# Kernel tuning notes

Measured on AMD Instinct MI355X. Metric: run time of the kernel, lower is better.

Reference implementation:

```python
import jax, jax.numpy as jnp
import numpy as np

PE_DIM = 64

def _layernorm(x, g, b, eps=1e-5):
    m = jnp.mean(x, -1, keepdims=True)
    v = jnp.mean((x - m) ** 2, -1, keepdims=True)
    return (x - m) * jax.lax.rsqrt(v + eps) * g + b

def _sinusoidal_pe(t, dim=PE_DIM):
    half = dim // 2
    freqs = jnp.exp(-jnp.log(10000.0) * jnp.arange(half) / half).astype(t.dtype)
    ang = t[..., None] * freqs  # [..., half]
    return jnp.concatenate([jnp.sin(ang), jnp.cos(ang)], -1)

def _bilinear(feats, b, t, x, y):
    # feats [B,Wl,H,W,D]; b,t int32 [B,Q,Wl,M] (b broadcastable); x,y in [0,1]
    # matches torch grid_sample(mode=bilinear, padding_mode=border, align_corners=False)
    H, W = feats.shape[2], feats.shape[3]
    px = x * W - 0.5
    py = y * H - 0.5
    x0 = jnp.floor(px); y0 = jnp.floor(py)
    wx = (px - x0)[..., None]; wy = (py - y0)[..., None]
    x0i = jnp.clip(x0.astype(jnp.int32), 0, W - 1)
    x1i = jnp.clip(x0.astype(jnp.int32) + 1, 0, W - 1)
    y0i = jnp.clip(y0.astype(jnp.int32), 0, H - 1)
    y1i = jnp.clip(y0.astype(jnp.int32) + 1, 0, H - 1)
    v00 = feats[b, t, y0i, x0i]  # [B,Q,Wl,M,D]
    v01 = feats[b, t, y0i, x1i]
    v10 = feats[b, t, y1i, x0i]
    v11 = feats[b, t, y1i, x1i]
    return (v00 * (1 - wy) * (1 - wx) + v01 * (1 - wy) * wx
            + v10 * wy * (1 - wx) + v11 * wy * wx)

def setup_inputs() -> dict:
    key = jax.random.key(0)
    ks = jax.random.split(key, 20)
    B, Q, Wl, H, W, D, M = 4, 300, 8, 64, 64, 256, 4
    s = 0.02
    inp = {
        'q': jax.random.normal(ks[0], (B, Q, D), jnp.float32),
        'kv_feats': jax.random.normal(ks[1], (B, Wl, H, W, D), jnp.float32),
        'kv_mask': jnp.zeros((B, Wl, H, W), jnp.bool_),
        'delta_sec': jax.random.normal(ks[2], (B, Q, Wl), jnp.float32),
        'w_ref': jax.random.normal(ks[3], (D, 2), jnp.float32) * s,
        'b_ref': jnp.zeros((2,), jnp.float32),
        'w_delta': jax.random.normal(ks[4], (2 * D, 3 * M), jnp.float32) * s,
        'b_delta': jnp.zeros((3 * M,), jnp.float32),
        'w_alpha': jax.random.normal(ks[5], (2 * D, M), jnp.float32) * s,
        'b_alpha': jnp.zeros((M,), jnp.float32),
        'lam': jnp.array(1.0, jnp.float32),
        'w_proj': jax.random.normal(ks[6], (D, D), jnp.float32) * s,
        'b_proj': jnp.zeros((D,), jnp.float32),
        'ln1_g': jnp.ones((D,), jnp.float32), 'ln1_b': jnp.zeros((D,), jnp.float32),
        'ln2_g': jnp.ones((D,), jnp.float32), 'ln2_b': jnp.zeros((D,), jnp.float32),
        'w_ffn1': jax.random.normal(ks[7], (D, 4 * D), jnp.float32) * s,
        'b_ffn1': jnp.zeros((4 * D,), jnp.float32),
        'w_ffn2': jax.random.normal(ks[8], (4 * D, D), jnp.float32) * s,
        'b_ffn2': jnp.zeros((D,), jnp.float32),
        'w_rel': jax.random.normal(ks[9], (PE_DIM, D), jnp.float32) * s,
        'b_rel': jnp.zeros((D,), jnp.float32),
    }
    return inp

def reference(q, kv_feats, kv_mask, delta_sec, w_ref, b_ref, w_delta, b_delta,
              w_alpha, b_alpha, lam, w_proj, b_proj, ln1_g, ln1_b, ln2_g, ln2_b,
              w_ffn1, b_ffn1, w_ffn2, b_ffn2, w_rel, b_rel):
    B, Q, D = q.shape
    Wl = kv_feats.shape[1]
    M = w_alpha.shape[1]

    qn = _layernorm(q, ln1_g, ln1_b)
    rel_feat = _sinusoidal_pe(delta_sec) @ w_rel + b_rel          # [B,Q,Wl,D]
    psi = jnp.concatenate([jnp.broadcast_to(qn[:, :, None, :], (B, Q, Wl, D)),
                           rel_feat], -1)                          # [B,Q,Wl,2D]

    delta = (psi @ w_delta + b_delta).reshape(B, Q, Wl, M, 3)
    logits = psi @ w_alpha + b_alpha                               # [B,Q,Wl,M]
    ref = jax.nn.sigmoid(qn @ w_ref + b_ref)                       # [B,Q,2]
    coords = ref[:, :, None, None, :] + jnp.tanh(delta[..., :2])   # [B,Q,Wl,M,2]
    coords = jnp.clip(coords, 0.0, 1.0)
    delta_t = jnp.tanh(delta[..., 2])                              # [B,Q,Wl,M]

    # mask features (mask==True -> invalid -> zero)
    feats = kv_feats * (~kv_mask)[..., None].astype(kv_feats.dtype)

    # temporal trilinear indices
    base = jnp.arange(Wl, dtype=q.dtype).reshape(1, 1, Wl, 1)
    target = base + delta_t
    t0f = jnp.clip(jnp.floor(target), 0, Wl - 1)
    t1f = jnp.clip(t0f + 1, 0, Wl - 1)
    alpha = (target - t0f)[..., None]
    t0 = t0f.astype(jnp.int32); t1 = t1f.astype(jnp.int32)

    bidx = jnp.arange(B, dtype=jnp.int32).reshape(B, 1, 1, 1)
    cx = coords[..., 0]; cy = coords[..., 1]
    s0 = _bilinear(feats, bidx, t0, cx, cy)                        # [B,Q,Wl,M,D]
    s1 = _bilinear(feats, bidx, t1, cx, cy)
    sampled = s0 * (1 - alpha) + s1 * alpha

    lam_sp = jax.nn.softplus(lam)
    weights = jax.nn.softmax(logits - lam_sp * jnp.abs(delta_sec)[..., None], axis=-1)
    agg = jnp.sum(weights[..., None] * sampled, axis=(2, 3))       # [B,Q,D]

    out = q + (agg @ w_proj + b_proj)
    h = _layernorm(out, ln2_g, ln2_b)
    ffn = jax.nn.gelu(h @ w_ffn1 + b_ffn1, approximate=False) @ w_ffn2 + b_ffn2
    return out + ffn
```

## Files before the change

### kernel.cpp

```cpp
#include <hip/hip_runtime.h>
#include <math.h>

#define Bn 4
#define Qn 300
#define WL 8
#define Hh 64
#define Ww 64
#define Dd 256
#define Mm 4

__device__ __forceinline__ float wave_reduce(float v) {
#pragma unroll
    for (int off = 32; off > 0; off >>= 1) v += __shfl_down(v, off, 64);
    return v;
}

__device__ __forceinline__ float block_reduce256(float v, float* lds) {
    v = wave_reduce(v);
    int lane = threadIdx.x & 63, wv = threadIdx.x >> 6;
    if (lane == 0) lds[wv] = v;
    __syncthreads();
    float r = lds[0] + lds[1] + lds[2] + lds[3];
    __syncthreads();
    return r;
}

__device__ __forceinline__ float lo16(unsigned u) { return __uint_as_float(u << 16); }
__device__ __forceinline__ float hi16(unsigned u) { return __uint_as_float(u & 0xffff0000u); }

__device__ __forceinline__ unsigned bfp(float a, float b) {
    unsigned ua = __float_as_uint(a); ua = (ua + 0x7fffu + ((ua >> 16) & 1u)) >> 16;
    unsigned ub = __float_as_uint(b); ub = (ub + 0x7fffu + ((ub >> 16) & 1u)) >> 16;
    return ua | (ub << 16);
}

__global__ void __launch_bounds__(256) k_mid(const float* __restrict__ wp,
                                             const float* __restrict__ wf1,
                                             const float* __restrict__ wf2,
                                             unsigned* __restrict__ pk,
                                             const float* __restrict__ q,
                                             const float* __restrict__ g1,
                                             const float* __restrict__ b1,
                                             const float* __restrict__ w_ref,
                                             const float* __restrict__ b_ref,
                                             const float* __restrict__ dsec,
                                             const float* __restrict__ w_rel,
                                             const float* __restrict__ b_rel,
                                             const float* __restrict__ w_delta,
                                             const float* __restrict__ b_delta,
                                             const float* __restrict__ w_alpha,
                                             const float* __restrict__ b_alpha,
                                             const unsigned char* __restrict__ mask,
                                             unsigned* __restrict__ prm2) {
    __shared__ float lds[4];
    __shared__ float sref[2];
    __shared__ float sqn[256];
    __shared__ float pe[8][64];
    __shared__ float rel[8][260];
    __shared__ float WcT[16 * 516];
    __shared__ float res[8][16];

    int bid = blockIdx.x, t = threadIdx.x;

    if (bid < 1152) {
        int i = bid * 256 + t;
        if (i < 32768) {
            int p = i & 3, c = (i >> 2) & 255, g = i >> 10;
            pk[i] = bfp(wp[(g * 8 + 2 * p) * 256 + c], wp[(g * 8 + 2 * p + 1) * 256 + c]);
        } else if (i < 163840) {
            int i2 = i - 32768;
            int p = i2 & 3, c = (i2 >> 2) & 1023, g = i2 >> 12;
            pk[i] = bfp(wf1[(g * 8 + 2 * p) * 1024 + c], wf1[(g * 8 + 2 * p + 1) * 1024 + c]);
        } else {
            int i3 = i - 163840;
            int p = i3 & 3, c = (i3 >> 2) & 255, g = i3 >> 10;
            pk[i] = bfp(wf2[(g * 8 + 2 * p) * 256 + c], wf2[(g * 8 + 2 * p + 1) * 256 + c]);
        }
        return;
    }

    int bq = bid - 1152;

    float x = q[bq * Dd + t];
    float m = block_reduce256(x, lds) * (1.f / Dd);
    float dx = x - m;
    float v = block_reduce256(dx * dx, lds) * (1.f / Dd);
    float y = dx * rsqrtf(v + 1e-5f) * g1[t] + b1[t];
    sqn[t] = y;

    float s0 = block_reduce256(y * w_ref[t * 2 + 0], lds);
    float s1 = block_reduce256(y * w_ref[t * 2 + 1], lds);
    if (t == 0) {
        sref[0] = 1.f / (1.f + expf(-(s0 + b_ref[0])));
        sref[1] = 1.f / (1.f + expf(-(s1 + b_ref[1])));
    }

    {
        int wl = t >> 5, i = t & 31;
        float f = expf(-logf(10000.f) * (float)i * (1.f / 32.f));
        float a = dsec[bq * WL + wl] * f;
        pe[wl][i] = sinf(a);
        pe[wl][i + 32] = cosf(a);
    }

    for (int u = t; u < 512 * 16; u += 256) {
        int k = u >> 4, jj = u & 15;
        float w = (jj < 12) ? w_delta[k * 12 + jj] : w_alpha[k * 4 + (jj - 12)];
        WcT[jj * 516 + k] = w;
    }

    float wr[64];
#pragma unroll
    for (int k = 0; k < 64; k++) wr[k] = w_rel[k * Dd + t];
    __syncthreads();

    float brl = b_rel[t];
    for (int wl = 0; wl < WL; wl++) {
        const float4* p4 = (const float4*)&pe[wl][0];
        float r = brl;
#pragma unroll
        for (int k4 = 0; k4 < 16; k4++) {
            float4 p = p4[k4];
            r += p.x * wr[4 * k4] + p.y * wr[4 * k4 + 1]
               + p.z * wr[4 * k4 + 2] + p.w * wr[4 * k4 + 3];
        }
        rel[wl][t] = r;
    }
    __syncthreads();

    if (t < 128) {
        int wl = t >> 4, jj = t & 15;
        const float4* wrow = (const float4*)&WcT[jj * 516];
        const float4* qrow = (const float4*)sqn;
        const float4* rrow = (const float4*)&rel[wl][0];
        float s = 0.f;
#pragma unroll 8
        for (int k4 = 0; k4 < 64; k4++) {
            float4 a = qrow[k4], w = wrow[k4];
            s += a.x * w.x + a.y * w.y + a.z * w.z + a.w * w.w;
        }
#pragma unroll 8
        for (int k4 = 0; k4 < 64; k4++) {
            float4 a = rrow[k4], w = wrow[64 + k4];
            s += a.x * w.x + a.y * w.y + a.z * w.z + a.w * w.w;
        }
        s += (jj < 12) ? b_delta[jj] : b_alpha[jj - 12];
        res[wl][jj] = s;
    }
    __syncthreads();

    if (t < 32) {
        int wl = t >> 2, mm = t & 3;
        float l0 = res[wl][12], l1 = res[wl][13], l2 = res[wl][14], l3 = res[wl][15];
        float mx = fmaxf(fmaxf(l0, l1), fmaxf(l2, l3));
        float inv = 1.f / (expf(l0 - mx) + expf(l1 - mx) + expf(l2 - mx) + expf(l3 - mx));
        float wgt = expf(res[wl][12 + mm] - mx) * inv;

        float cx = fminf(fmaxf(sref[0] + tanhf(res[wl][mm * 3 + 0]), 0.f), 1.f);
        float cy = fminf(fmaxf(sref[1] + tanhf(res[wl][mm * 3 + 1]), 0.f), 1.f);
        float tgt = (float)wl + tanhf(res[wl][mm * 3 + 2]);
        float t0f = fminf(fmaxf(floorf(tgt), 0.f), (float)(WL - 1));
        float t1f = fminf(t0f + 1.f, (float)(WL - 1));
        float alpha = tgt - t0f;
        float px = cx * (float)Ww - 0.5f, py = cy * (float)Hh - 0.5f;
        float fx = floorf(px), fy = floorf(py);
        float wx = px - fx, wy = py - fy;
        int X0 = (int)fminf(fmaxf(fx, 0.f), (float)(Ww - 1));
        int X1 = (int)fminf(fmaxf(fx + 1.f, 0.f), (float)(Ww - 1));
        int Y0 = (int)fminf(fmaxf(fy, 0.f), (float)(Hh - 1));
        int Y1 = (int)fminf(fmaxf(fy + 1.f, 0.f), (float)(Hh - 1));
        int T0 = (int)t0f, T1 = (int)t1f;

        float w00 = (1.f - wy) * (1.f - wx), w01 = (1.f - wy) * wx;
        float w10 = wy * (1.f - wx), w11 = wy * wx;
        float wt0 = wgt * (1.f - alpha), wt1 = wgt * alpha;

        int b = bq / Qn;
        int base0 = (b * WL + T0) * Hh;
        int base1 = (b * WL + T1) * Hh;
        int i00 = (base0 + Y0) * Ww + X0, i01 = (base0 + Y0) * Ww + X1;
        int i10 = (base0 + Y1) * Ww + X0, i11 = (base0 + Y1) * Ww + X1;
        int j00 = (base1 + Y0) * Ww + X0, j01 = (base1 + Y0) * Ww + X1;
        int j10 = (base1 + Y1) * Ww + X0, j11 = (base1 + Y1) * Ww + X1;

        unsigned* rec = prm2 + (unsigned)(bq * 32 + t) * 16;
        rec[0] = __float_as_uint(wt0 * w00 * (mask[i00] ? 0.f : 1.f));
        rec[1] = __float_as_uint(wt0 * w01 * (mask[i01] ? 0.f : 1.f));
        rec[2] = __float_as_uint(wt0 * w10 * (mask[i10] ? 0.f : 1.f));
        rec[3] = __float_as_uint(wt0 * w11 * (mask[i11] ? 0.f : 1.f));
        rec[4] = __float_as_uint(wt1 * w00 * (mask[j00] ? 0.f : 1.f));
        rec[5] = __float_as_uint(wt1 * w01 * (mask[j01] ? 0.f : 1.f));
        rec[6] = __float_as_uint(wt1 * w10 * (mask[j10] ? 0.f : 1.f));
        rec[7] = __float_as_uint(wt1 * w11 * (mask[j11] ? 0.f : 1.f));
        rec[8] = i00; rec[9] = i01; rec[10] = i10; rec[11] = i11;
        rec[12] = j00; rec[13] = j01; rec[14] = j10; rec[15] = j11;
    }
}

__global__ void __launch_bounds__(512) k_gather(const float* __restrict__ feats,
                                                const unsigned* __restrict__ prm2,
                                                float* __restrict__ agg) {
    __shared__ unsigned P[32 * 16];
    __shared__ float part[8][256];
    int bq = blockIdx.x, t = threadIdx.x;
    int l = t & 63, j = t >> 6;
    P[t] = prm2[(unsigned)bq * 512 + t];
    __syncthreads();
    const float4* f4 = (const float4*)feats;
    float4 acc = {0.f, 0.f, 0.f, 0.f};
#pragma unroll
    for (int p = 0; p < 4; p++) {
        const unsigned* rec = &P[(j * 4 + p) * 16];
#pragma unroll
        for (int cn = 0; cn < 8; cn++) {
            float w = __uint_as_float(rec[cn]);
            size_t idx = rec[8 + cn];
            float4 v = f4[idx * 64 + l];
            acc.x += w * v.x; acc.y += w * v.y; acc.z += w * v.z; acc.w += w * v.w;
        }
    }
    ((float4*)&part[j][0])[l] = acc;
    __syncthreads();
    if (t < 256) {
        float s = part[0][t] + part[1][t] + part[2][t] + part[3][t]
                + part[4][t] + part[5][t] + part[6][t] + part[7][t];
        agg[(size_t)bq * Dd + t] = s;
    }
}

template<int R>
__device__ __forceinline__ void out_body(int row0,
        const float* __restrict__ q, const float* __restrict__ agg,
        const unsigned* __restrict__ pkP, const float* __restrict__ b_proj,
        const float* __restrict__ g2, const float* __restrict__ b2,
        const unsigned* __restrict__ pkF1, const float* __restrict__ b_ffn1,
        const unsigned* __restrict__ pkF2, const float* __restrict__ b_ffn2,
        float* __restrict__ out,
        float* sA, float* sO, float* sH, float* sF, float* sP, float* sRed) {
    int t = threadIdx.x;
    int c = t & 255, j = t >> 8;

    for (int u = t; u < 256 * R; u += 1024) {
        int r = u >> 8, cc = u & 255;
        sA[r * 256 + cc] = agg[(size_t)(row0 + r) * Dd + cc];
    }
    __syncthreads();

    {
        float acc[R];
#pragma unroll
        for (int r = 0; r < R; r++) acc[r] = 0.f;
#pragma unroll 2
        for (int gg = 0; gg < 8; gg++) {
            int g = j * 8 + gg;
            uint4 wv = *(const uint4*)&pkP[((unsigned)(g * 256 + c)) * 4];
            float w0 = lo16(wv.x), w1 = hi16(wv.x), w2 = lo16(wv.y), w3 = hi16(wv.y);
            float w4 = lo16(wv.z), w5 = hi16(wv.z), w6 = lo16(wv.w), w7 = hi16(wv.w);
#pragma unroll
            for (int r = 0; r < R; r++) {
                float4 ha = ((const float4*)&sA[r * 256])[g * 2];
                float4 hb = ((const float4*)&sA[r * 256])[g * 2 + 1];
                acc[r] += ha.x * w0 + ha.y * w1 + ha.z * w2 + ha.w * w3
                        + hb.x * w4 + hb.y * w5 + hb.z * w6 + hb.w * w7;
            }
        }
#pragma unroll
        for (int r = 0; r < R; r++) sP[(j * 5 + r) * 256 + c] = acc[r];
    }
    __syncthreads();

    for (int u = t; u < 256 * R; u += 1024) {
        int r = u >> 8, cc = u & 255;
        float o = sP[(0 * 5 + r) * 256 + cc] + sP[(1 * 5 + r) * 256 + cc]
                + sP[(2 * 5 + r) * 256 + cc] + sP[(3 * 5 + r) * 256 + cc]
                + q[(size_t)(row0 + r) * Dd + cc] + b_proj[cc];
        sO[r * 256 + cc] = o;
    }
    __syncthreads();

    {
        int wv = t >> 6, l = t & 63;
        if (wv < R) {
            float4 v = ((const float4*)&sO[wv * 256])[l];
            float s = v.x + v.y + v.z + v.w;
            s = __shfl(wave_reduce(s), 0, 64);
            float mean = s * (1.f / 256.f);
            float d0 = v.x - mean, d1 = v.y - mean, d2 = v.z - mean, d3 = v.w - mean;
            float ss = d0 * d0 + d1 * d1 + d2 * d2 + d3 * d3;
            ss = __shfl(wave_reduce(ss), 0, 64);
            float rstd = rsqrtf(ss * (1.f / 256.f) + 1e-5f);
            if (l == 0) { sRed[wv * 2] = mean; sRed[wv * 2 + 1] = rstd; }
        }
    }
    __syncthreads();
    for (int u = t; u < 256 * R; u += 1024) {
        int r = u >> 8, cc = u & 255;
        sH[r * 256 + cc] = (sO[r * 256 + cc] - sRed[r * 2]) * sRed[r * 2 + 1] * g2[cc] + b2[cc];
    }
    __syncthreads();

    {
        float f[R];
#pragma unroll
        for (int r = 0; r < R; r++) f[r] = 0.f;
#pragma unroll 2
        for (int g = 0; g < 32; g++) {
            uint4 wv = *(const uint4*)&pkF1[((unsigned)(g * 1024 + t)) * 4];
            float w0 = lo16(wv.x), w1 = hi16(wv.x), w2 = lo16(wv.y), w3 = hi16(wv.y);
            float w4 = lo16(wv.z), w5 = hi16(wv.z), w6 = lo16(wv.w), w7 = hi16(wv.w);
#pragma unroll
            for (int r = 0; r < R; r++) {
                float4 ha = ((const float4*)&sH[r * 256])[g * 2];
                float4 hb = ((const float4*)&sH[r * 256])[g * 2 + 1];
                f[r] += ha.x * w0 + ha.y * w1 + ha.z * w2 + ha.w * w3
                      + hb.x * w4 + hb.y * w5 + hb.z * w6 + hb.w * w7;
            }
        }
        float bf = b_ffn1[t];
#pragma unroll
        for (int r = 0; r < R; r++) {
            float xx = f[r] + bf;
            sF[r * 1024 + t] = 0.5f * xx * (1.f + erff(xx * 0.70710678118654752f));
        }
    }
    __syncthreads();

    {
        float acc[R];
#pragma unroll
        for (int r = 0; r < R; r++) acc[r] = 0.f;
#pragma unroll 2
        for (int gg = 0; gg < 32; gg++) {
            int g = j * 32 + gg;
            uint4 wv = *(const uint4*)&pkF2[((unsigned)(g * 256 + c)) * 4];
            float w0 = lo16(wv.x), w1 = hi16(wv.x), w2 = lo16(wv.y), w3 = hi16(wv.y);
            float w4 = lo16(wv.z), w5 = hi16(wv.z), w6 = lo16(wv.w), w7 = hi16(wv.w);
#pragma unroll
            for (int r = 0; r < R; r++) {
                float4 ha = ((const float4*)&sF[r * 1024])[g * 2];
                float4 hb = ((const float4*)&sF[r * 1024])[g * 2 + 1];
                acc[r] += ha.x * w0 + ha.y * w1 + ha.z * w2 + ha.w * w3
                        + hb.x * w4 + hb.y * w5 + hb.z * w6 + hb.w * w7;
            }
        }
#pragma unroll
        for (int r = 0; r < R; r++) sP[(j * 5 + r) * 256 + c] = acc[r];
    }
    __syncthreads();

    for (int u = t; u < 256 * R; u += 1024) {
        int r = u >> 8, cc = u & 255;
        float s = sP[(0 * 5 + r) * 256 + cc] + sP[(1 * 5 + r) * 256 + cc]
                + sP[(2 * 5 + r) * 256 + cc] + sP[(3 * 5 + r) * 256 + cc];
        out[(size_t)(row0 + r) * Dd + cc] = sO[r * 256 + cc] + s + b_ffn2[cc];
    }
}

__global__ void __launch_bounds__(1024) k_out(const float* __restrict__ q,
                                              const float* __restrict__ agg,
                                              const unsigned* __restrict__ pkP,
                                              const float* __restrict__ b_proj,
                                              const float* __restrict__ g2,
                                              const float* __restrict__ b2,
                                              const unsigned* __restrict__ pkF1,
                                              const float* __restrict__ b_ffn1,
                                              const unsigned* __restrict__ pkF2,
                                              const float* __restrict__ b_ffn2,
                                              float* __restrict__ out) {
    __shared__ float sA[5 * 256];
    __shared__ float sO[5 * 256];
    __shared__ float sH[5 * 256];
    __shared__ float sF[5 * 1024];
    __shared__ float sP[4 * 5 * 256];
    __shared__ float sRed[16];
    __shared__ float pad[8192];
    if (b_ffn2 == nullptr) pad[threadIdx.x] = 0.f;

    int bid = blockIdx.x;
    if (bid < 176) {
        out_body<5>(bid * 5, q, agg, pkP, b_proj, g2, b2, pkF1, b_ffn1, pkF2, b_ffn2,
                    out, sA, sO, sH, sF, sP, sRed);
    } else {
        out_body<4>(880 + (bid - 176) * 4, q, agg, pkP, b_proj, g2, b2, pkF1, b_ffn1,
                    pkF2, b_ffn2, out, sA, sO, sH, sF, sP, sRed);
    }
}

extern "C" void kernel_launch(void* const* d_in, const int* in_sizes, int n_in,
                              void* d_out, int out_size, void* d_ws, size_t ws_size,
                              hipStream_t stream) {
    const float* q        = (const float*)d_in[0];
    const float* kv_feats = (const float*)d_in[1];
    const unsigned char* kv_mask = (const unsigned char*)d_in[2];
    const float* delta_sec= (const float*)d_in[3];
    const float* w_ref    = (const float*)d_in[4];
    const float* b_ref    = (const float*)d_in[5];
    const float* w_delta  = (const float*)d_in[6];
    const float* b_delta  = (const float*)d_in[7];
    const float* w_alpha  = (const float*)d_in[8];
    const float* b_alpha  = (const float*)d_in[9];
    const float* w_proj   = (const float*)d_in[11];
    const float* b_proj   = (const float*)d_in[12];
    const float* ln1_g    = (const float*)d_in[13];
    const float* ln1_b    = (const float*)d_in[14];
    const float* ln2_g    = (const float*)d_in[15];
    const float* ln2_b    = (const float*)d_in[16];
    const float* w_ffn1   = (const float*)d_in[17];
    const float* b_ffn1   = (const float*)d_in[18];
    const float* w_ffn2   = (const float*)d_in[19];
    const float* b_ffn2   = (const float*)d_in[20];
    const float* w_rel    = (const float*)d_in[21];
    const float* b_rel    = (const float*)d_in[22];
    float* out = (float*)d_out;

    unsigned* pk   = (unsigned*)d_ws;
    unsigned* pkP  = pk;
    unsigned* pkF1 = pk + 32768;
    unsigned* pkF2 = pk + 163840;
    unsigned* prm2 = pk + 294912;
    float*    agg  = (float*)(prm2 + 614400);

    const int BQ = Bn * Qn;
    k_mid<<<dim3(1152 + BQ), dim3(256), 0, stream>>>(w_proj, w_ffn1, w_ffn2, pk,
                                                     q, ln1_g, ln1_b, w_ref, b_ref,
                                                     delta_sec, w_rel, b_rel,
                                                     w_delta, b_delta, w_alpha, b_alpha,
                                                     kv_mask, prm2);
    k_gather<<<dim3(BQ), dim3(512), 0, stream>>>(kv_feats, prm2, agg);
    k_out<<<dim3(256), dim3(1024), 0, stream>>>(q, agg, pkP, b_proj, ln2_g, ln2_b,
                                                pkF1, b_ffn1, pkF2, b_ffn2, out);
}
```

Baseline: 300.8 us.

## Fuse sampling-parameter and gather kernels; split k_out matmul work into two-column threads

```diff
diff --git a/kernel.cpp b/kernel.cpp
--- a/kernel.cpp
+++ b/kernel.cpp
@@ -15,16 +15,6 @@
     return v;
 }
 
-__device__ __forceinline__ float block_reduce256(float v, float* lds) {
-    v = wave_reduce(v);
-    int lane = threadIdx.x & 63, wv = threadIdx.x >> 6;
-    if (lane == 0) lds[wv] = v;
-    __syncthreads();
-    float r = lds[0] + lds[1] + lds[2] + lds[3];
-    __syncthreads();
-    return r;
-}
-
 __device__ __forceinline__ float lo16(unsigned u) { return __uint_as_float(u << 16); }
 __device__ __forceinline__ float hi16(unsigned u) { return __uint_as_float(u & 0xffff0000u); }
 
@@ -34,36 +24,39 @@
     return ua | (ub << 16);
 }
 
-__global__ void __launch_bounds__(256) k_mid(const float* __restrict__ wp,
-                                             const float* __restrict__ wf1,
-                                             const float* __restrict__ wf2,
-                                             unsigned* __restrict__ pk,
-                                             const float* __restrict__ q,
-                                             const float* __restrict__ g1,
-                                             const float* __restrict__ b1,
-                                             const float* __restrict__ w_ref,
-                                             const float* __restrict__ b_ref,
-                                             const float* __restrict__ dsec,
-                                             const float* __restrict__ w_rel,
-                                             const float* __restrict__ b_rel,
-                                             const float* __restrict__ w_delta,
-                                             const float* __restrict__ b_delta,
-                                             const float* __restrict__ w_alpha,
-                                             const float* __restrict__ b_alpha,
-                                             const unsigned char* __restrict__ mask,
-                                             unsigned* __restrict__ prm2) {
-    __shared__ float lds[4];
-    __shared__ float sref[2];
-    __shared__ float sqn[256];
-    __shared__ float pe[8][64];
-    __shared__ float rel[8][260];
-    __shared__ float WcT[16 * 516];
-    __shared__ float res[8][16];
-
+__device__ __forceinline__ void unpack8(uint4 wv, float* w) {
+    w[0] = lo16(wv.x); w[1] = hi16(wv.x); w[2] = lo16(wv.y); w[3] = hi16(wv.y);
+    w[4] = lo16(wv.z); w[5] = hi16(wv.z); w[6] = lo16(wv.w); w[7] = hi16(wv.w);
+}
+
+__device__ __forceinline__ float dot8(float4 ha, float4 hb, const float* w) {
+    return ha.x * w[0] + ha.y * w[1] + ha.z * w[2] + ha.w * w[3]
+         + hb.x * w[4] + hb.y * w[5] + hb.z * w[6] + hb.w * w[7];
+}
+
+__global__ void __launch_bounds__(512, 4) k_front(const float* __restrict__ wp,
+                                                  const float* __restrict__ wf1,
+                                                  const float* __restrict__ wf2,
+                                                  unsigned* __restrict__ pk,
+                                                  const float* __restrict__ q,
+                                                  const float* __restrict__ g1,
+                                                  const float* __restrict__ b1,
+                                                  const float* __restrict__ w_ref,
+                                                  const float* __restrict__ b_ref,
+                                                  const float* __restrict__ dsec,
+                                                  const float* __restrict__ w_rel,
+                                                  const float* __restrict__ b_rel,
+                                                  const float* __restrict__ w_delta,
+                                                  const float* __restrict__ b_delta,
+                                                  const float* __restrict__ w_alpha,
+                                                  const float* __restrict__ b_alpha,
+                                                  const unsigned char* __restrict__ mask,
+                                                  const float* __restrict__ feats,
+                                                  float* __restrict__ agg) {
     int bid = blockIdx.x, t = threadIdx.x;
 
-    if (bid < 1152) {
-        int i = bid * 256 + t;
+    if (bid < 576) {
+        int i = bid * 512 + t;
         if (i < 32768) {
             int p = i & 3, c = (i >> 2) & 255, g = i >> 10;
             pk[i] = bfp(wp[(g * 8 + 2 * p) * 256 + c], wp[(g * 8 + 2 * p + 1) * 256 + c]);
@@ -79,73 +72,103 @@
         return;
     }
 
-    int bq = bid - 1152;
-
-    float x = q[bq * Dd + t];
-    float m = block_reduce256(x, lds) * (1.f / Dd);
-    float dx = x - m;
-    float v = block_reduce256(dx * dx, lds) * (1.f / Dd);
-    float y = dx * rsqrtf(v + 1e-5f) * g1[t] + b1[t];
-    sqn[t] = y;
-
-    float s0 = block_reduce256(y * w_ref[t * 2 + 0], lds);
-    float s1 = block_reduce256(y * w_ref[t * 2 + 1], lds);
-    if (t == 0) {
-        sref[0] = 1.f / (1.f + expf(-(s0 + b_ref[0])));
-        sref[1] = 1.f / (1.f + expf(-(s1 + b_ref[1])));
-    }
-
-    {
-        int wl = t >> 5, i = t & 31;
-        float f = expf(-logf(10000.f) * (float)i * (1.f / 32.f));
-        float a = dsec[bq * WL + wl] * f;
-        pe[wl][i] = sinf(a);
-        pe[wl][i + 32] = cosf(a);
-    }
-
-    for (int u = t; u < 512 * 16; u += 256) {
+    __shared__ float sqn[256];
+    __shared__ float pe[8][64];
+    __shared__ float rel[8][260];
+    __shared__ float WcT[16 * 516];
+    __shared__ float dres[2][8][16];
+    __shared__ float res[8][16];
+    __shared__ float red[16];
+    __shared__ float sref[2];
+    __shared__ unsigned Prec[32 * 16];
+    __shared__ float part[8][256];
+
+    int bq = bid - 576;
+    int ch = t & 255;
+    bool lo = t < 256;
+    int lane = t & 63, wv = t >> 6;
+
+    float wr[64];
+#pragma unroll
+    for (int k = 0; k < 64; k++) wr[k] = w_rel[k * Dd + ch];
+
+    for (int u = t; u < 512 * 16; u += 512) {
         int k = u >> 4, jj = u & 15;
         float w = (jj < 12) ? w_delta[k * 12 + jj] : w_alpha[k * 4 + (jj - 12)];
         WcT[jj * 516 + k] = w;
     }
 
-    float wr[64];
-#pragma unroll
-    for (int k = 0; k < 64; k++) wr[k] = w_rel[k * Dd + t];
-    __syncthreads();
-
-    float brl = b_rel[t];
-    for (int wl = 0; wl < WL; wl++) {
-        const float4* p4 = (const float4*)&pe[wl][0];
-        float r = brl;
-#pragma unroll
-        for (int k4 = 0; k4 < 16; k4++) {
-            float4 p = p4[k4];
-            r += p.x * wr[4 * k4] + p.y * wr[4 * k4 + 1]
-               + p.z * wr[4 * k4 + 2] + p.w * wr[4 * k4 + 3];
-        }
-        rel[wl][t] = r;
-    }
-    __syncthreads();
-
-    if (t < 128) {
-        int wl = t >> 4, jj = t & 15;
-        const float4* wrow = (const float4*)&WcT[jj * 516];
-        const float4* qrow = (const float4*)sqn;
-        const float4* rrow = (const float4*)&rel[wl][0];
+    float x = lo ? q[bq * Dd + ch] : 0.f;
+    float sm = wave_reduce(x);
+    if (lane == 0) red[wv] = sm;
+    __syncthreads();
+    float m = (red[0] + red[1] + red[2] + red[3] + red[4] + red[5] + red[6] + red[7]) * (1.f / Dd);
+    __syncthreads();
+    float dx = lo ? (x - m) : 0.f;
+    float sv = wave_reduce(dx * dx);
+    if (lane == 0) red[wv] = sv;
+    __syncthreads();
+    float v = (red[0] + red[1] + red[2] + red[3] + red[4] + red[5] + red[6] + red[7]) * (1.f / Dd);
+    __syncthreads();
+    float y = 0.f;
+    if (lo) { y = dx * rsqrtf(v + 1e-5f) * g1[ch] + b1[ch]; sqn[ch] = y; }
+
+    if (lo) {
+        int wl = t >> 5, i2 = t & 31;
+        float f = expf(-logf(10000.f) * (float)i2 * (1.f / 32.f));
+        float a = dsec[bq * WL + wl] * f;
+        pe[wl][i2] = sinf(a);
+        pe[wl][i2 + 32] = cosf(a);
+    }
+
+    float c0 = lo ? y * w_ref[2 * ch] : 0.f;
+    float c1 = lo ? y * w_ref[2 * ch + 1] : 0.f;
+    c0 = wave_reduce(c0); c1 = wave_reduce(c1);
+    if (lane == 0) { red[wv] = c0; red[8 + wv] = c1; }
+    __syncthreads();
+    if (t == 0) {
+        float s0 = red[0] + red[1] + red[2] + red[3] + red[4] + red[5] + red[6] + red[7] + b_ref[0];
+        float s1 = red[8] + red[9] + red[10] + red[11] + red[12] + red[13] + red[14] + red[15] + b_ref[1];
+        sref[0] = 1.f / (1.f + expf(-s0));
+        sref[1] = 1.f / (1.f + expf(-s1));
+    }
+
+    {
+        float brl = b_rel[ch];
+        int wh = t >> 8;
+#pragma unroll
+        for (int w2 = 0; w2 < 4; w2++) {
+            int wl = wh * 4 + w2;
+            const float4* p4 = (const float4*)&pe[wl][0];
+            float r = brl;
+#pragma unroll
+            for (int k4 = 0; k4 < 16; k4++) {
+                float4 p = p4[k4];
+                r += p.x * wr[4 * k4] + p.y * wr[4 * k4 + 1]
+                   + p.z * wr[4 * k4 + 2] + p.w * wr[4 * k4 + 3];
+            }
+            rel[wl][ch] = r;
+        }
+    }
+    __syncthreads();
+
+    if (t < 256) {
+        int h = t >> 7, idx = t & 127, wl = idx >> 4, jj = idx & 15;
+        const float4* wrow = (const float4*)&WcT[jj * 516 + h * 256];
+        const float4* arow = h ? (const float4*)&rel[wl][0] : (const float4*)sqn;
         float s = 0.f;
 #pragma unroll 8
         for (int k4 = 0; k4 < 64; k4++) {
-            float4 a = qrow[k4], w = wrow[k4];
+            float4 a = arow[k4], w = wrow[k4];
             s += a.x * w.x + a.y * w.y + a.z * w.z + a.w * w.w;
         }
-#pragma unroll 8
-        for (int k4 = 0; k4 < 64; k4++) {
-            float4 a = rrow[k4], w = wrow[64 + k4];
-            s += a.x * w.x + a.y * w.y + a.z * w.z + a.w * w.w;
-        }
-        s += (jj < 12) ? b_delta[jj] : b_alpha[jj - 12];
-        res[wl][jj] = s;
+        dres[h][wl][jj] = s;
+    }
+    __syncthreads();
+    if (t < 128) {
+        int wl = t >> 4, jj = t & 15;
+        res[wl][jj] = dres[0][wl][jj] + dres[1][wl][jj]
+                    + ((jj < 12) ? b_delta[jj] : b_alpha[jj - 12]);
     }
     __syncthreads();
 
@@ -183,7 +206,7 @@
         int j00 = (base1 + Y0) * Ww + X0, j01 = (base1 + Y0) * Ww + X1;
         int j10 = (base1 + Y1) * Ww + X0, j11 = (base1 + Y1) * Ww + X1;
 
-        unsigned* rec = prm2 + (unsigned)(bq * 32 + t) * 16;
+        unsigned* rec = &Prec[t * 16];
         rec[0] = __float_as_uint(wt0 * w00 * (mask[i00] ? 0.f : 1.f));
         rec[1] = __float_as_uint(wt0 * w01 * (mask[i01] ? 0.f : 1.f));
         rec[2] = __float_as_uint(wt0 * w10 * (mask[i10] ? 0.f : 1.f));
@@ -195,36 +218,29 @@
         rec[8] = i00; rec[9] = i01; rec[10] = i10; rec[11] = i11;
         rec[12] = j00; rec[13] = j01; rec[14] = j10; rec[15] = j11;
     }
-}
-
-__global__ void __launch_bounds__(512) k_gather(const float* __restrict__ feats,
-                                                const unsigned* __restrict__ prm2,
-                                                float* __restrict__ agg) {
-    __shared__ unsigned P[32 * 16];
-    __shared__ float part[8][256];
-    int bq = blockIdx.x, t = threadIdx.x;
-    int l = t & 63, j = t >> 6;
-    P[t] = prm2[(unsigned)bq * 512 + t];
-    __syncthreads();
-    const float4* f4 = (const float4*)feats;
-    float4 acc = {0.f, 0.f, 0.f, 0.f};
-#pragma unroll
-    for (int p = 0; p < 4; p++) {
-        const unsigned* rec = &P[(j * 4 + p) * 16];
-#pragma unroll
-        for (int cn = 0; cn < 8; cn++) {
-            float w = __uint_as_float(rec[cn]);
-            size_t idx = rec[8 + cn];
-            float4 v = f4[idx * 64 + l];
-            acc.x += w * v.x; acc.y += w * v.y; acc.z += w * v.z; acc.w += w * v.w;
-        }
-    }
-    ((float4*)&part[j][0])[l] = acc;
+    __syncthreads();
+
+    {
+        const float4* f4 = (const float4*)feats;
+        int j = t >> 6;
+        float4 acc = {0.f, 0.f, 0.f, 0.f};
+#pragma unroll
+        for (int p = 0; p < 4; p++) {
+            const unsigned* rec = &Prec[(j * 4 + p) * 16];
+#pragma unroll
+            for (int cn = 0; cn < 8; cn++) {
+                float w = __uint_as_float(rec[cn]);
+                size_t idx = rec[8 + cn];
+                float4 vv = f4[idx * 64 + lane];
+                acc.x += w * vv.x; acc.y += w * vv.y; acc.z += w * vv.z; acc.w += w * vv.w;
+            }
+        }
+        ((float4*)&part[j][0])[lane] = acc;
+    }
     __syncthreads();
     if (t < 256) {
-        float s = part[0][t] + part[1][t] + part[2][t] + part[3][t]
-                + part[4][t] + part[5][t] + part[6][t] + part[7][t];
-        agg[(size_t)bq * Dd + t] = s;
+        agg[(size_t)bq * Dd + t] = part[0][t] + part[1][t] + part[2][t] + part[3][t]
+                                 + part[4][t] + part[5][t] + part[6][t] + part[7][t];
     }
 }
 
@@ -236,9 +252,9 @@
         const unsigned* __restrict__ pkF1, const float* __restrict__ b_ffn1,
         const unsigned* __restrict__ pkF2, const float* __restrict__ b_ffn2,
         float* __restrict__ out,
-        float* sA, float* sO, float* sH, float* sF, float* sP, float* sRed) {
+        float* sA, float* sO, float* sH, float* sF, float* sX, float* sRed) {
     int t = threadIdx.x;
-    int c = t & 255, j = t >> 8;
+    int j8 = t >> 7, c7 = t & 127;
 
     for (int u = t; u < 256 * R; u += 1024) {
         int r = u >> 8, cc = u & 255;
@@ -247,33 +263,35 @@
     __syncthreads();
 
     {
-        float acc[R];
-#pragma unroll
-        for (int r = 0; r < R; r++) acc[r] = 0.f;
-#pragma unroll 2
-        for (int gg = 0; gg < 8; gg++) {
-            int g = j * 8 + gg;
-            uint4 wv = *(const uint4*)&pkP[((unsigned)(g * 256 + c)) * 4];
-            float w0 = lo16(wv.x), w1 = hi16(wv.x), w2 = lo16(wv.y), w3 = hi16(wv.y);
-            float w4 = lo16(wv.z), w5 = hi16(wv.z), w6 = lo16(wv.w), w7 = hi16(wv.w);
+        float a0[R], a1[R];
+#pragma unroll
+        for (int r = 0; r < R; r++) { a0[r] = 0.f; a1[r] = 0.f; }
+#pragma unroll
+        for (int gg = 0; gg < 4; gg++) {
+            int g = j8 * 4 + gg;
+            uint4 wv0 = *(const uint4*)&pkP[((unsigned)(g * 256 + c7)) * 4];
+            uint4 wv1 = *(const uint4*)&pkP[((unsigned)(g * 256 + c7 + 128)) * 4];
+            float w0[8], w1[8]; unpack8(wv0, w0); unpack8(wv1, w1);
 #pragma unroll
             for (int r = 0; r < R; r++) {
                 float4 ha = ((const float4*)&sA[r * 256])[g * 2];
                 float4 hb = ((const float4*)&sA[r * 256])[g * 2 + 1];
-                acc[r] += ha.x * w0 + ha.y * w1 + ha.z * w2 + ha.w * w3
-                        + hb.x * w4 + hb.y * w5 + hb.z * w6 + hb.w * w7;
+                a0[r] += dot8(ha, hb, w0); a1[r] += dot8(ha, hb, w1);
             }
         }
 #pragma unroll
-        for (int r = 0; r < R; r++) sP[(j * 5 + r) * 256 + c] = acc[r];
+        for (int r = 0; r < R; r++) {
+            sX[(j8 * R + r) * 256 + c7] = a0[r];
+            sX[(j8 * R + r) * 256 + c7 + 128] = a1[r];
+        }
     }
     __syncthreads();
 
     for (int u = t; u < 256 * R; u += 1024) {
         int r = u >> 8, cc = u & 255;
-        float o = sP[(0 * 5 + r) * 256 + cc] + sP[(1 * 5 + r) * 256 + cc]
-                + sP[(2 * 5 + r) * 256 + cc] + sP[(3 * 5 + r) * 256 + cc]
-                + q[(size_t)(row0 + r) * Dd + cc] + b_proj[cc];
+        float o = q[(size_t)(row0 + r) * Dd + cc] + b_proj[cc];
+#pragma unroll
+        for (int jj = 0; jj < 8; jj++) o += sX[(jj * R + r) * 256 + cc];
         sO[r * 256 + cc] = o;
     }
     __syncthreads();
@@ -281,11 +299,11 @@
     {
         int wv = t >> 6, l = t & 63;
         if (wv < R) {
-            float4 v = ((const float4*)&sO[wv * 256])[l];
-            float s = v.x + v.y + v.z + v.w;
+            float4 vv = ((const float4*)&sO[wv * 256])[l];
+            float s = vv.x + vv.y + vv.z + vv.w;
             s = __shfl(wave_reduce(s), 0, 64);
             float mean = s * (1.f / 256.f);
-            float d0 = v.x - mean, d1 = v.y - mean, d2 = v.z - mean, d3 = v.w - mean;
+            float d0 = vv.x - mean, d1 = vv.y - mean, d2 = vv.z - mean, d3 = vv.w - mean;
             float ss = d0 * d0 + d1 * d1 + d2 * d2 + d3 * d3;
             ss = __shfl(wave_reduce(ss), 0, 64);
             float rstd = rsqrtf(ss * (1.f / 256.f) + 1e-5f);
@@ -300,59 +318,72 @@
     __syncthreads();
 
     {
-        float f[R];
-#pragma unroll
-        for (int r = 0; r < R; r++) f[r] = 0.f;
+        int h = t >> 9, c2 = t & 511;
+        float f0[R], f1[R];
+#pragma unroll
+        for (int r = 0; r < R; r++) { f0[r] = 0.f; f1[r] = 0.f; }
 #pragma unroll 2
-        for (int g = 0; g < 32; g++) {
-            uint4 wv = *(const uint4*)&pkF1[((unsigned)(g * 1024 + t)) * 4];
-            float w0 = lo16(wv.x), w1 = hi16(wv.x), w2 = lo16(wv.y), w3 = hi16(wv.y);
-            float w4 = lo16(wv.z), w5 = hi16(wv.z), w6 = lo16(wv.w), w7 = hi16(wv.w);
+        for (int gg = 0; gg < 16; gg++) {
+            int g = h * 16 + gg;
+            uint4 wv0 = *(const uint4*)&pkF1[((unsigned)(g * 1024 + c2)) * 4];
+            uint4 wv1 = *(const uint4*)&pkF1[((unsigned)(g * 1024 + c2 + 512)) * 4];
+            float w0[8], w1[8]; unpack8(wv0, w0); unpack8(wv1, w1);
 #pragma unroll
             for (int r = 0; r < R; r++) {
                 float4 ha = ((const float4*)&sH[r * 256])[g * 2];
                 float4 hb = ((const float4*)&sH[r * 256])[g * 2 + 1];
-                f[r] += ha.x * w0 + ha.y * w1 + ha.z * w2 + ha.w * w3
-                      + hb.x * w4 + hb.y * w5 + hb.z * w6 + hb.w * w7;
+                f0[r] += dot8(ha, hb, w0); f1[r] += dot8(ha, hb, w1);
             }
         }
+        float* dst = sX + h * (R * 1024);
+#pragma unroll
+        for (int r = 0; r < R; r++) {
+            dst[r * 1024 + c2] = f0[r];
+            dst[r * 1024 + c2 + 512] = f1[r];
+        }
+    }
+    __syncthreads();
+    {
         float bf = b_ffn1[t];
 #pragma unroll
         for (int r = 0; r < R; r++) {
-            float xx = f[r] + bf;
+            float xx = sX[r * 1024 + t] + sX[R * 1024 + r * 1024 + t] + bf;
             sF[r * 1024 + t] = 0.5f * xx * (1.f + erff(xx * 0.70710678118654752f));
         }
     }
     __syncthreads();
 
     {
-        float acc[R];
-#pragma unroll
-        for (int r = 0; r < R; r++) acc[r] = 0.f;
+        float a0[R], a1[R];
+#pragma unroll
+        for (int r = 0; r < R; r++) { a0[r] = 0.f; a1[r] = 0.f; }
 #pragma unroll 2
-        for (int gg = 0; gg < 32; gg++) {
-            int g = j * 32 + gg;
-            uint4 wv = *(const uint4*)&pkF2[((unsigned)(g * 256 + c)) * 4];
-            float w0 = lo16(wv.x), w1 = hi16(wv.x), w2 = lo16(wv.y), w3 = hi16(wv.y);
-            float w4 = lo16(wv.z), w5 = hi16(wv.z), w6 = lo16(wv.w), w7 = hi16(wv.w);
+        for (int gg = 0; gg < 16; gg++) {
+            int g = j8 * 16 + gg;
+            uint4 wv0 = *(const uint4*)&pkF2[((unsigned)(g * 256 + c7)) * 4];
+            uint4 wv1 = *(const uint4*)&pkF2[((unsigned)(g * 256 + c7 + 128)) * 4];
+            float w0[8], w1[8]; unpack8(wv0, w0); unpack8(wv1, w1);
 #pragma unroll
             for (int r = 0; r < R; r++) {
                 float4 ha = ((const float4*)&sF[r * 1024])[g * 2];
                 float4 hb = ((const float4*)&sF[r * 1024])[g * 2 + 1];
-                acc[r] += ha.x * w0 + ha.y * w1 + ha.z * w2 + ha.w * w3
-                        + hb.x * w4 + hb.y * w5 + hb.z * w6 + hb.w * w7;
+                a0[r] += dot8(ha, hb, w0); a1[r] += dot8(ha, hb, w1);
             }
         }
 #pragma unroll
-        for (int r = 0; r < R; r++) sP[(j * 5 + r) * 256 + c] = acc[r];
+        for (int r = 0; r < R; r++) {
+            sX[(j8 * R + r) * 256 + c7] = a0[r];
+            sX[(j8 * R + r) * 256 + c7 + 128] = a1[r];
+        }
     }
     __syncthreads();
 
     for (int u = t; u < 256 * R; u += 1024) {
         int r = u >> 8, cc = u & 255;
-        float s = sP[(0 * 5 + r) * 256 + cc] + sP[(1 * 5 + r) * 256 + cc]
-                + sP[(2 * 5 + r) * 256 + cc] + sP[(3 * 5 + r) * 256 + cc];
-        out[(size_t)(row0 + r) * Dd + cc] = sO[r * 256 + cc] + s + b_ffn2[cc];
+        float s = b_ffn2[cc];
+#pragma unroll
+        for (int jj = 0; jj < 8; jj++) s += sX[(jj * R + r) * 256 + cc];
+        out[(size_t)(row0 + r) * Dd + cc] = sO[r * 256 + cc] + s;
     }
 }
 
@@ -371,18 +402,18 @@
     __shared__ float sO[5 * 256];
     __shared__ float sH[5 * 256];
     __shared__ float sF[5 * 1024];
-    __shared__ float sP[4 * 5 * 256];
+    __shared__ float sX[10240];
     __shared__ float sRed[16];
-    __shared__ float pad[8192];
-    if (b_ffn2 == nullptr) pad[threadIdx.x] = 0.f;
+    __shared__ float pad[1600];
+    if (b_ffn2 == nullptr) pad[threadIdx.x & 1023] = 0.f;
 
     int bid = blockIdx.x;
     if (bid < 176) {
         out_body<5>(bid * 5, q, agg, pkP, b_proj, g2, b2, pkF1, b_ffn1, pkF2, b_ffn2,
-                    out, sA, sO, sH, sF, sP, sRed);
+                    out, sA, sO, sH, sF, sX, sRed);
     } else {
         out_body<4>(880 + (bid - 176) * 4, q, agg, pkP, b_proj, g2, b2, pkF1, b_ffn1,
-                    pkF2, b_ffn2, out, sA, sO, sH, sF, sP, sRed);
+                    pkF2, b_ffn2, out, sA, sO, sH, sF, sX, sRed);
     }
 }
 
@@ -417,16 +448,14 @@
     unsigned* pkP  = pk;
     unsigned* pkF1 = pk + 32768;
     unsigned* pkF2 = pk + 163840;
-    unsigned* prm2 = pk + 294912;
-    float*    agg  = (float*)(prm2 + 614400);
+    float*    agg  = (float*)(pk + 294912);
 
     const int BQ = Bn * Qn;
-    k_mid<<<dim3(1152 + BQ), dim3(256), 0, stream>>>(w_proj, w_ffn1, w_ffn2, pk,
-                                                     q, ln1_g, ln1_b, w_ref, b_ref,
-                                                     delta_sec, w_rel, b_rel,
-                                                     w_delta, b_delta, w_alpha, b_alpha,
-                                                     kv_mask, prm2);
-    k_gather<<<dim3(BQ), dim3(512), 0, stream>>>(kv_feats, prm2, agg);
+    k_front<<<dim3(576 + BQ), dim3(512), 0, stream>>>(w_proj, w_ffn1, w_ffn2, pk,
+                                                      q, ln1_g, ln1_b, w_ref, b_ref,
+                                                      delta_sec, w_rel, b_rel,
+                                                      w_delta, b_delta, w_alpha, b_alpha,
+                                                      kv_mask, kv_feats, agg);
     k_out<<<dim3(256), dim3(1024), 0, stream>>>(q, agg, pkP, b_proj, ln2_g, ln2_b,
                                                 pkF1, b_ffn1, pkF2, b_ffn2, out);
 }
```

Result: no change. 299.1 us (-0.5%).
